# Kernel optimization log

Hardware: AMD Instinct MI355X
Metric: run time of the kernel (lower is better)

The kernel has to match this reference:

```python
import jax, jax.numpy as jnp
import numpy as np

S = 256      # batch == seq_len (required by the module's einsum index aliasing)
E = 1024     # emb_size
H = 16       # num_heads
D = E // H   # head dim
SCALE = float(np.sqrt(E))  # applied AFTER softmax, as in the original


def setup_inputs() -> dict:
    key = jax.random.key(0)
    ks = jax.random.split(key, 9)
    std = 1.0 / float(np.sqrt(E))
    lin = lambda k: jax.random.uniform(k, (E, E), jnp.float32, -std, std)
    b = lambda k: jax.random.uniform(k, (E,), jnp.float32, -std, std)
    return {
        "x": jax.random.normal(ks[0], (S, S, E), jnp.float32),
        "Wq": lin(ks[1]), "bq": b(jax.random.fold_in(ks[1], 1)),
        "Wk": lin(ks[2]), "bk": b(jax.random.fold_in(ks[2], 1)),
        "Wv": lin(ks[3]), "bv": b(jax.random.fold_in(ks[3], 1)),
        "Wp": lin(ks[4]), "bp": b(jax.random.fold_in(ks[4], 1)),
    }


def reference(x, Wq, bq, Wk, bk, Wv, bv, Wp, bp):
    # Linear projections (torch Linear: y = x @ W.T + b), split into heads.
    q = (x @ Wq.T + bq).reshape(S, S, H, D)  # (i, j, h, d)
    k = (x @ Wk.T + bk).reshape(S, S, H, D)
    v = (x @ Wv.T + bv).reshape(S, S, H, D)
    # Faithful to torch.einsum('bhqd,hbkd->bhqk', Q, K): K's leading two axes
    # are read transposed relative to Q, giving an HxH head-vs-head score map
    # per (i, j) token pair.
    energy = jnp.einsum('ijqd,jikd->ijqk', q, k)          # (S, S, H, H)
    # softmax over the QUERY-head axis (dim=2), then scale (post-softmax!)
    att = jax.nn.softmax(energy, axis=2) / SCALE
    # torch.einsum('bhal,bhlv->bhav', att, V)
    out = jnp.einsum('ijal,ijlv->ijav', att, v).reshape(S, S, E)
    return out @ Wp.T + bp
```

## Files before the change

kernel.cpp:

```cpp
#include <hip/hip_runtime.h>
#include <stdint.h>

#define KK_  1024

typedef __bf16 bf16x8 __attribute__((ext_vector_type(8)));
typedef float  f32x4  __attribute__((ext_vector_type(4)));
typedef unsigned short u16x8 __attribute__((ext_vector_type(8)));

__device__ __forceinline__ void cp16(void* lds, const void* g) {
  __builtin_amdgcn_global_load_lds(
      (const __attribute__((address_space(1))) void*)g,
      (__attribute__((address_space(3))) void*)lds, 16, 0, 0);
}

__device__ __forceinline__ float b2f(unsigned short u) {
  union { unsigned int i; float f; } x;
  x.i = ((unsigned int)u) << 16;
  return x.f;
}

__device__ __forceinline__ unsigned short f2b(float f) {
  unsigned int u = __builtin_bit_cast(unsigned int, f);
  unsigned int lsb = (u >> 16) & 1u;
  u += 0x7fffu + lsb;
  return (unsigned short)(u >> 16);
}

__global__ __launch_bounds__(256) void cvt_f32_bf16(
    const float* __restrict__ src, unsigned short* __restrict__ dst, int n) {
  int i = (blockIdx.x * 256 + threadIdx.x) * 4;
  if (i < n) {
    float4 v = *(const float4*)(src + i);
    ushort4 r;
    r.x = f2b(v.x); r.y = f2b(v.y); r.z = f2b(v.z); r.w = f2b(v.w);
    *(ushort4*)(dst + i) = r;
  }
}

template <bool OUT_F32>
__global__ __launch_bounds__(256) void gemm_bt(
    const unsigned short* __restrict__ A,
    const unsigned short* __restrict__ W0,
    const unsigned short* __restrict__ W1,
    const unsigned short* __restrict__ W2,
    const float* __restrict__ b0,
    const float* __restrict__ b1,
    const float* __restrict__ b2,
    void* __restrict__ Cout,
    int Nout) {
  __shared__ __align__(16) unsigned short sA[128 * 64];
  __shared__ __align__(16) unsigned short sB[128 * 64];

  const int t  = threadIdx.x;
  const int bx = blockIdx.x;
  const int by = blockIdx.y;
  const int wsel = by >> 3;
  const int nloc = (by & 7) * 128;
  const unsigned short* Wm = (wsel == 0) ? W0 : ((wsel == 1) ? W1 : W2);
  const float* bias        = (wsel == 0) ? b0 : ((wsel == 1) ? b1 : b2);

  const int ar = t >> 3;
  const int ac = ((t & 7) * 8) ^ ((ar & 7) * 8);
  const unsigned short* gA = A  + (size_t)(bx * 128 + ar) * KK_ + ac;
  const unsigned short* gB = Wm + (size_t)(nloc + ar) * KK_ + ac;

  const int lane = t & 63;
  const int wv = t >> 6;
  const int wm = (wv >> 1) * 64;
  const int wn = (wv & 1) * 64;
  const int fr = lane & 15;
  const int fk = (lane >> 4) * 8;
  const int swz = (fr & 7) << 4;

  f32x4 zero = {0.f, 0.f, 0.f, 0.f};
  f32x4 acc[4][4];
#pragma unroll
  for (int a = 0; a < 4; ++a)
#pragma unroll
    for (int b = 0; b < 4; ++b) acc[a][b] = zero;

  for (int k0 = 0; k0 < KK_; k0 += 64) {
#pragma unroll
    for (int it = 0; it < 4; ++it) {
      cp16(sA + t * 8 + it * 2048, gA + (size_t)it * 32 * KK_ + k0);
      cp16(sB + t * 8 + it * 2048, gB + (size_t)it * 32 * KK_ + k0);
    }
    __syncthreads();

#pragma unroll
    for (int kk = 0; kk < 64; kk += 32) {
      bf16x8 af[4], bfv[4];
#pragma unroll
      for (int mt = 0; mt < 4; ++mt)
        af[mt] = *(const bf16x8*)((const unsigned char*)sA +
            ((((wm + mt * 16 + fr) * 64 + kk + fk) * 2) ^ swz));
#pragma unroll
      for (int nt = 0; nt < 4; ++nt)
        bfv[nt] = *(const bf16x8*)((const unsigned char*)sB +
            ((((wn + nt * 16 + fr) * 64 + kk + fk) * 2) ^ swz));
#pragma unroll
      for (int mt = 0; mt < 4; ++mt)
#pragma unroll
        for (int nt = 0; nt < 4; ++nt)
          acc[mt][nt] = __builtin_amdgcn_mfma_f32_16x16x32_bf16(
              af[mt], bfv[nt], acc[mt][nt], 0, 0, 0);
    }
    __syncthreads();
  }

  const int cc = lane & 15;
  const int rq = (lane >> 4) * 4;
#pragma unroll
  for (int mt = 0; mt < 4; ++mt) {
#pragma unroll
    for (int nt = 0; nt < 4; ++nt) {
      const int gn = by * 128 + wn + nt * 16 + cc;
      const float bb = bias[nloc + wn + nt * 16 + cc];
#pragma unroll
      for (int r = 0; r < 4; ++r) {
        const int gm = bx * 128 + wm + mt * 16 + rq + r;
        const float val = acc[mt][nt][r] + bb;
        if (OUT_F32)
          ((float*)Cout)[(size_t)gm * Nout + gn] = val;
        else
          ((unsigned short*)Cout)[(size_t)gm * Nout + gn] = f2b(val);
      }
    }
  }
}

__global__ __launch_bounds__(256) void attn_wave(
    const unsigned short* __restrict__ qkv,
    unsigned short* __restrict__ ao) {
  const int lane = threadIdx.x & 63;
  const int p = blockIdx.x * 4 + (threadIdx.x >> 6);
  const int i = p >> 8;
  const int j = p & 255;

  const unsigned short* q = qkv + (size_t)p * 3072;
  const unsigned short* k = qkv + (size_t)(j * 256 + i) * 3072 + 1024;
  const unsigned short* v = q + 2048;

  const int fr = lane & 15;
  const int g  = lane >> 4;
  const int fk = g * 8;

  const bf16x8 kf0 = *(const bf16x8*)(k + fr * 64 + fk);
  const bf16x8 kf1 = *(const bf16x8*)(k + fr * 64 + 32 + fk);
  const bf16x8 qf0 = *(const bf16x8*)(q + fr * 64 + fk);
  const bf16x8 qf1 = *(const bf16x8*)(q + fr * 64 + 32 + fk);

  f32x4 e = {0.f, 0.f, 0.f, 0.f};
  e = __builtin_amdgcn_mfma_f32_16x16x32_bf16(kf0, qf0, e, 0, 0, 0);
  e = __builtin_amdgcn_mfma_f32_16x16x32_bf16(kf1, qf1, e, 0, 0, 0);

  float att[4];
#pragma unroll
  for (int r = 0; r < 4; ++r) {
    float m = e[r];
#pragma unroll
    for (int mask = 1; mask <= 8; mask <<= 1)
      m = fmaxf(m, __shfl_xor(m, mask));
    const float pe = __expf(e[r] - m);
    float s = pe;
#pragma unroll
    for (int mask = 1; mask <= 8; mask <<= 1)
      s += __shfl_xor(s, mask);
    att[r] = pe / (32.0f * s);
  }

  const int c0 = g * 16;
  float o[16];
#pragma unroll
  for (int u = 0; u < 16; ++u) o[u] = 0.f;

#pragma unroll
  for (int kh = 0; kh < 16; ++kh) {
    const float w = __shfl(att[kh & 3], fr + (kh >> 2) * 16);
    const u16x8 v0 = *(const u16x8*)(v + kh * 64 + c0);
    const u16x8 v1 = *(const u16x8*)(v + kh * 64 + c0 + 8);
#pragma unroll
    for (int u = 0; u < 8; ++u) {
      o[u]     += w * b2f(v0[u]);
      o[8 + u] += w * b2f(v1[u]);
    }
  }

  u16x8 r0, r1;
#pragma unroll
  for (int u = 0; u < 8; ++u) { r0[u] = f2b(o[u]); r1[u] = f2b(o[8 + u]); }
  unsigned short* dst = ao + (size_t)p * 1024 + fr * 64 + c0;
  *(u16x8*)dst       = r0;
  *(u16x8*)(dst + 8) = r1;
}

extern "C" void kernel_launch(void* const* d_in, const int* in_sizes, int n_in,
                              void* d_out, int out_size, void* d_ws, size_t ws_size,
                              hipStream_t stream) {
  const float* x  = (const float*)d_in[0];
  const float* Wq = (const float*)d_in[1];
  const float* bq = (const float*)d_in[2];
  const float* Wk = (const float*)d_in[3];
  const float* bk = (const float*)d_in[4];
  const float* Wv = (const float*)d_in[5];
  const float* bv = (const float*)d_in[6];
  const float* Wp = (const float*)d_in[7];
  const float* bp = (const float*)d_in[8];
  float* out = (float*)d_out;

  unsigned short* qkv     = (unsigned short*)d_ws;
  unsigned short* ao      = qkv + (size_t)65536 * 3072;
  unsigned short* Wqkv_bf = ao  + (size_t)65536 * 1024;
  unsigned short* Wp_bf   = Wqkv_bf + (size_t)3072 * 1024;
  unsigned short* x_bf = (unsigned short*)d_out;

  const int NX = 65536 * 1024;
  const int NW = 1024 * 1024;

  cvt_f32_bf16<<<NX / 1024, 256, 0, stream>>>(x, x_bf, NX);
  cvt_f32_bf16<<<NW / 1024, 256, 0, stream>>>(Wq, Wqkv_bf, NW);
  cvt_f32_bf16<<<NW / 1024, 256, 0, stream>>>(Wk, Wqkv_bf + (size_t)NW, NW);
  cvt_f32_bf16<<<NW / 1024, 256, 0, stream>>>(Wv, Wqkv_bf + (size_t)2 * NW, NW);
  cvt_f32_bf16<<<NW / 1024, 256, 0, stream>>>(Wp, Wp_bf, NW);

  gemm_bt<false><<<dim3(512, 24), dim3(256), 0, stream>>>(
      x_bf, Wqkv_bf, Wqkv_bf + (size_t)NW, Wqkv_bf + (size_t)2 * NW,
      bq, bk, bv, (void*)qkv, 3072);
  attn_wave<<<dim3(65536 / 4), dim3(256), 0, stream>>>(qkv, ao);
  gemm_bt<true><<<dim3(512, 8), dim3(256), 0, stream>>>(
      ao, Wp_bf, Wp_bf, Wp_bf, bp, bp, bp, (void*)out, 1024);
}
```

Measured before the change: 1.410 ms.

## Double-buffer GEMM LDS tiles and remap workgroups for XCD-aware cache reuse

The GEMM kernel now uses two LDS buffers, issuing the async global-to-LDS loads for the next K slice before computing on the current one, with one barrier per iteration instead of two. The grid is transposed so N tiles vary fastest, and the flat block index is permuted across the 8 XCDs so blocks that share an A row tile land on the same XCD and reuse it from L2. LDS use doubles to 64KB per block, which may lower occupancy.

```diff
diff --git a/kernel.cpp b/kernel.cpp
--- a/kernel.cpp
+++ b/kernel.cpp
@@ -48,20 +48,25 @@
     const float* __restrict__ b2,
     void* __restrict__ Cout,
     int Nout) {
-  __shared__ __align__(16) unsigned short sA[128 * 64];
-  __shared__ __align__(16) unsigned short sB[128 * 64];
+  __shared__ __align__(16) unsigned short sA[2][128 * 64];
+  __shared__ __align__(16) unsigned short sB[2][128 * 64];
 
   const int t  = threadIdx.x;
-  const int bx = blockIdx.x;
-  const int by = blockIdx.y;
-  const int wsel = by >> 3;
-  const int nloc = (by & 7) * 128;
+  const int NT   = gridDim.x;
+  const int nwg  = NT * gridDim.y;
+  const int flat = blockIdx.y * NT + blockIdx.x;
+  const int wg   = (flat & 7) * (nwg >> 3) + (flat >> 3);
+  const int ntile = wg % NT;
+  const int mtile = wg / NT;
+
+  const int wsel = ntile >> 3;
+  const int nloc = (ntile & 7) * 128;
   const unsigned short* Wm = (wsel == 0) ? W0 : ((wsel == 1) ? W1 : W2);
   const float* bias        = (wsel == 0) ? b0 : ((wsel == 1) ? b1 : b2);
 
   const int ar = t >> 3;
   const int ac = ((t & 7) * 8) ^ ((ar & 7) * 8);
-  const unsigned short* gA = A  + (size_t)(bx * 128 + ar) * KK_ + ac;
+  const unsigned short* gA = A  + (size_t)(mtile * 128 + ar) * KK_ + ac;
   const unsigned short* gB = Wm + (size_t)(nloc + ar) * KK_ + ac;
 
   const int lane = t & 63;
@@ -79,24 +84,25 @@
 #pragma unroll
     for (int b = 0; b < 4; ++b) acc[a][b] = zero;
 
-  for (int k0 = 0; k0 < KK_; k0 += 64) {
+  auto stage = [&](int buf, int k0) {
 #pragma unroll
     for (int it = 0; it < 4; ++it) {
-      cp16(sA + t * 8 + it * 2048, gA + (size_t)it * 32 * KK_ + k0);
-      cp16(sB + t * 8 + it * 2048, gB + (size_t)it * 32 * KK_ + k0);
-    }
-    __syncthreads();
-
+      cp16(&sA[buf][t * 8 + it * 2048], gA + (size_t)it * 32 * KK_ + k0);
+      cp16(&sB[buf][t * 8 + it * 2048], gB + (size_t)it * 32 * KK_ + k0);
+    }
+  };
+
+  auto compute = [&](int buf) {
 #pragma unroll
     for (int kk = 0; kk < 64; kk += 32) {
       bf16x8 af[4], bfv[4];
 #pragma unroll
       for (int mt = 0; mt < 4; ++mt)
-        af[mt] = *(const bf16x8*)((const unsigned char*)sA +
+        af[mt] = *(const bf16x8*)((const unsigned char*)sA[buf] +
             ((((wm + mt * 16 + fr) * 64 + kk + fk) * 2) ^ swz));
 #pragma unroll
       for (int nt = 0; nt < 4; ++nt)
-        bfv[nt] = *(const bf16x8*)((const unsigned char*)sB +
+        bfv[nt] = *(const bf16x8*)((const unsigned char*)sB[buf] +
             ((((wn + nt * 16 + fr) * 64 + kk + fk) * 2) ^ swz));
 #pragma unroll
       for (int mt = 0; mt < 4; ++mt)
@@ -105,8 +111,18 @@
           acc[mt][nt] = __builtin_amdgcn_mfma_f32_16x16x32_bf16(
               af[mt], bfv[nt], acc[mt][nt], 0, 0, 0);
     }
+  };
+
+  stage(0, 0);
+  __syncthreads();
+  int cur = 0;
+  for (int k0 = 64; k0 < KK_; k0 += 64) {
+    stage(cur ^ 1, k0);
+    compute(cur);
     __syncthreads();
-  }
+    cur ^= 1;
+  }
+  compute(cur);
 
   const int cc = lane & 15;
   const int rq = (lane >> 4) * 4;
@@ -114,11 +130,11 @@
   for (int mt = 0; mt < 4; ++mt) {
 #pragma unroll
     for (int nt = 0; nt < 4; ++nt) {
-      const int gn = by * 128 + wn + nt * 16 + cc;
+      const int gn = ntile * 128 + wn + nt * 16 + cc;
       const float bb = bias[nloc + wn + nt * 16 + cc];
 #pragma unroll
       for (int r = 0; r < 4; ++r) {
-        const int gm = bx * 128 + wm + mt * 16 + rq + r;
+        const int gm = mtile * 128 + wm + mt * 16 + rq + r;
         const float val = acc[mt][nt][r] + bb;
         if (OUT_F32)
           ((float*)Cout)[(size_t)gm * Nout + gn] = val;
@@ -223,10 +239,10 @@
   cvt_f32_bf16<<<NW / 1024, 256, 0, stream>>>(Wv, Wqkv_bf + (size_t)2 * NW, NW);
   cvt_f32_bf16<<<NW / 1024, 256, 0, stream>>>(Wp, Wp_bf, NW);
 
-  gemm_bt<false><<<dim3(512, 24), dim3(256), 0, stream>>>(
+  gemm_bt<false><<<dim3(24, 512), dim3(256), 0, stream>>>(
       x_bf, Wqkv_bf, Wqkv_bf + (size_t)NW, Wqkv_bf + (size_t)2 * NW,
       bq, bk, bv, (void*)qkv, 3072);
   attn_wave<<<dim3(65536 / 4), dim3(256), 0, stream>>>(qkv, ao);
-  gemm_bt<true><<<dim3(512, 8), dim3(256), 0, stream>>>(
+  gemm_bt<true><<<dim3(8, 512), dim3(256), 0, stream>>>(
       ao, Wp_bf, Wp_bf, Wp_bf, bp, bp, bp, (void*)out, 1024);
 }
```

Result: no change. 1.419 ms (+0.7%).

## Make attention waves persistent with prefetch, split QKV GEMM into three launches

Applied to the files above, without the earlier changes.

The attention kernel now launches 2048 blocks, and each wave handles 8 token pairs strided by 8192. It prefetches the next pair's Q/K fragments and keeps a rolling 4-deep buffer of V loads, so memory latency overlaps with the softmax and weighted-sum work. The fused QKV GEMM is split into three separate launches, one per weight, with an output column offset, which removes the per-block weight and bias selection. This adds launch overhead and per-wave register pressure, and leaves an unused dead code block in the attention kernel.

```diff
diff --git a/kernel.cpp b/kernel.cpp
--- a/kernel.cpp
+++ b/kernel.cpp
@@ -40,12 +40,8 @@
 template <bool OUT_F32>
 __global__ __launch_bounds__(256) void gemm_bt(
     const unsigned short* __restrict__ A,
-    const unsigned short* __restrict__ W0,
-    const unsigned short* __restrict__ W1,
-    const unsigned short* __restrict__ W2,
-    const float* __restrict__ b0,
-    const float* __restrict__ b1,
-    const float* __restrict__ b2,
+    const unsigned short* __restrict__ Wm,
+    const float* __restrict__ bias,
     void* __restrict__ Cout,
     int Nout) {
   __shared__ __align__(16) unsigned short sA[128 * 64];
@@ -54,10 +50,7 @@
   const int t  = threadIdx.x;
   const int bx = blockIdx.x;
   const int by = blockIdx.y;
-  const int wsel = by >> 3;
-  const int nloc = (by & 7) * 128;
-  const unsigned short* Wm = (wsel == 0) ? W0 : ((wsel == 1) ? W1 : W2);
-  const float* bias        = (wsel == 0) ? b0 : ((wsel == 1) ? b1 : b2);
+  const int nloc = by * 128;
 
   const int ar = t >> 3;
   const int ac = ((t & 7) * 8) ^ ((ar & 7) * 8);
@@ -133,65 +126,98 @@
     const unsigned short* __restrict__ qkv,
     unsigned short* __restrict__ ao) {
   const int lane = threadIdx.x & 63;
-  const int p = blockIdx.x * 4 + (threadIdx.x >> 6);
-  const int i = p >> 8;
-  const int j = p & 255;
-
-  const unsigned short* q = qkv + (size_t)p * 3072;
-  const unsigned short* k = qkv + (size_t)(j * 256 + i) * 3072 + 1024;
-  const unsigned short* v = q + 2048;
+  const int w = blockIdx.x * 4 + (threadIdx.x >> 6);
 
   const int fr = lane & 15;
   const int g  = lane >> 4;
   const int fk = g * 8;
-
-  const bf16x8 kf0 = *(const bf16x8*)(k + fr * 64 + fk);
-  const bf16x8 kf1 = *(const bf16x8*)(k + fr * 64 + 32 + fk);
-  const bf16x8 qf0 = *(const bf16x8*)(q + fr * 64 + fk);
-  const bf16x8 qf1 = *(const bf16x8*)(q + fr * 64 + 32 + fk);
-
-  f32x4 e = {0.f, 0.f, 0.f, 0.f};
-  e = __builtin_amdgcn_mfma_f32_16x16x32_bf16(kf0, qf0, e, 0, 0, 0);
-  e = __builtin_amdgcn_mfma_f32_16x16x32_bf16(kf1, qf1, e, 0, 0, 0);
-
-  float att[4];
-#pragma unroll
-  for (int r = 0; r < 4; ++r) {
-    float m = e[r];
-#pragma unroll
-    for (int mask = 1; mask <= 8; mask <<= 1)
-      m = fmaxf(m, __shfl_xor(m, mask));
-    const float pe = __expf(e[r] - m);
-    float s = pe;
-#pragma unroll
-    for (int mask = 1; mask <= 8; mask <<= 1)
-      s += __shfl_xor(s, mask);
-    att[r] = pe / (32.0f * s);
-  }
-
   const int c0 = g * 16;
-  float o[16];
-#pragma unroll
-  for (int u = 0; u < 16; ++u) o[u] = 0.f;
-
-#pragma unroll
-  for (int kh = 0; kh < 16; ++kh) {
-    const float w = __shfl(att[kh & 3], fr + (kh >> 2) * 16);
-    const u16x8 v0 = *(const u16x8*)(v + kh * 64 + c0);
-    const u16x8 v1 = *(const u16x8*)(v + kh * 64 + c0 + 8);
-#pragma unroll
-    for (int u = 0; u < 8; ++u) {
-      o[u]     += w * b2f(v0[u]);
-      o[8 + u] += w * b2f(v1[u]);
-    }
-  }
-
-  u16x8 r0, r1;
-#pragma unroll
-  for (int u = 0; u < 8; ++u) { r0[u] = f2b(o[u]); r1[u] = f2b(o[8 + u]); }
-  unsigned short* dst = ao + (size_t)p * 1024 + fr * 64 + c0;
-  *(u16x8*)dst       = r0;
-  *(u16x8*)(dst + 8) = r1;
+
+  int p = w;
+  {
+    const unsigned short* q0 = qkv + (size_t)p * 3072;
+    const unsigned short* k0 =
+        qkv + (size_t)(((p & 255) << 8) + (p >> 8)) * 3072 + 1024;
+  }
+  const unsigned short* qp = qkv + (size_t)p * 3072;
+  const unsigned short* kp =
+      qkv + (size_t)(((p & 255) << 8) + (p >> 8)) * 3072 + 1024;
+  bf16x8 kf0 = *(const bf16x8*)(kp + fr * 64 + fk);
+  bf16x8 kf1 = *(const bf16x8*)(kp + fr * 64 + 32 + fk);
+  bf16x8 qf0 = *(const bf16x8*)(qp + fr * 64 + fk);
+  bf16x8 qf1 = *(const bf16x8*)(qp + fr * 64 + 32 + fk);
+
+  for (int it = 0; it < 8; ++it) {
+    const unsigned short* v = qkv + (size_t)p * 3072 + 2048;
+    unsigned short* dst = ao + (size_t)p * 1024 + fr * 64 + c0;
+    const int pn = p + 8192;
+
+    const bf16x8 ckf0 = kf0, ckf1 = kf1, cqf0 = qf0, cqf1 = qf1;
+
+    if (it < 7) {
+      const unsigned short* qn = qkv + (size_t)pn * 3072;
+      const unsigned short* kn =
+          qkv + (size_t)(((pn & 255) << 8) + (pn >> 8)) * 3072 + 1024;
+      kf0 = *(const bf16x8*)(kn + fr * 64 + fk);
+      kf1 = *(const bf16x8*)(kn + fr * 64 + 32 + fk);
+      qf0 = *(const bf16x8*)(qn + fr * 64 + fk);
+      qf1 = *(const bf16x8*)(qn + fr * 64 + 32 + fk);
+    }
+
+    u16x8 va[4], vb[4];
+#pragma unroll
+    for (int kh = 0; kh < 4; ++kh) {
+      va[kh] = *(const u16x8*)(v + kh * 64 + c0);
+      vb[kh] = *(const u16x8*)(v + kh * 64 + c0 + 8);
+    }
+
+    f32x4 e = {0.f, 0.f, 0.f, 0.f};
+    e = __builtin_amdgcn_mfma_f32_16x16x32_bf16(ckf0, cqf0, e, 0, 0, 0);
+    e = __builtin_amdgcn_mfma_f32_16x16x32_bf16(ckf1, cqf1, e, 0, 0, 0);
+
+    float att[4];
+#pragma unroll
+    for (int r = 0; r < 4; ++r) {
+      float m = e[r];
+#pragma unroll
+      for (int mask = 1; mask <= 8; mask <<= 1)
+        m = fmaxf(m, __shfl_xor(m, mask));
+      const float pe = __expf(e[r] - m);
+      float s = pe;
+#pragma unroll
+      for (int mask = 1; mask <= 8; mask <<= 1)
+        s += __shfl_xor(s, mask);
+      att[r] = pe / (32.0f * s);
+    }
+
+    float o[16];
+#pragma unroll
+    for (int u = 0; u < 16; ++u) o[u] = 0.f;
+
+#pragma unroll
+    for (int kh = 0; kh < 16; ++kh) {
+      const u16x8 v0 = va[kh & 3];
+      const u16x8 v1 = vb[kh & 3];
+      if (kh < 12) {
+        va[kh & 3] = *(const u16x8*)(v + (kh + 4) * 64 + c0);
+        vb[kh & 3] = *(const u16x8*)(v + (kh + 4) * 64 + c0 + 8);
+      }
+      const float wgt = __shfl(att[kh & 3], fr + (kh >> 2) * 16);
+#pragma unroll
+      for (int u = 0; u < 8; ++u) {
+        o[u]     += wgt * b2f(v0[u]);
+        o[8 + u] += wgt * b2f(v1[u]);
+      }
+    }
+
+    u16x8 r0, r1;
+#pragma unroll
+    for (int u = 0; u < 8; ++u) { r0[u] = f2b(o[u]); r1[u] = f2b(o[8 + u]); }
+    *(u16x8*)dst       = r0;
+    *(u16x8*)(dst + 8) = r1;
+
+    p = pn;
+  }
 }
 
 extern "C" void kernel_launch(void* const* d_in, const int* in_sizes, int n_in,
@@ -223,10 +249,15 @@
   cvt_f32_bf16<<<NW / 1024, 256, 0, stream>>>(Wv, Wqkv_bf + (size_t)2 * NW, NW);
   cvt_f32_bf16<<<NW / 1024, 256, 0, stream>>>(Wp, Wp_bf, NW);
 
-  gemm_bt<false><<<dim3(512, 24), dim3(256), 0, stream>>>(
-      x_bf, Wqkv_bf, Wqkv_bf + (size_t)NW, Wqkv_bf + (size_t)2 * NW,
-      bq, bk, bv, (void*)qkv, 3072);
-  attn_wave<<<dim3(65536 / 4), dim3(256), 0, stream>>>(qkv, ao);
+  gemm_bt<false><<<dim3(512, 8), dim3(256), 0, stream>>>(
+      x_bf, Wqkv_bf, bq, (void*)qkv, 3072);
+  gemm_bt<false><<<dim3(512, 8), dim3(256), 0, stream>>>(
+      x_bf, Wqkv_bf + (size_t)NW, bk, (void*)(qkv + 1024), 3072);
+  gemm_bt<false><<<dim3(512, 8), dim3(256), 0, stream>>>(
+      x_bf, Wqkv_bf + (size_t)2 * NW, bv, (void*)(qkv + 2048), 3072);
+
+  attn_wave<<<dim3(2048), dim3(256), 0, stream>>>(qkv, ao);
+
   gemm_bt<true><<<dim3(512, 8), dim3(256), 0, stream>>>(
-      ao, Wp_bf, Wp_bf, Wp_bf, bp, bp, bp, (void*)out, 1024);
-}
+      ao, Wp_bf, bp, (void*)out, 1024);
+}
```

Result: no change. 1.437 ms (+1.9%).
